# Performance work log

Measured on AMD Instinct MI355X. Metric: run time of the kernel, lower is better.

Reference implementation:

```python
import jax, jax.numpy as jnp
import numpy as np

D_MODEL = 2048
N_HEADS = 16
HEAD_DIM = D_MODEL // N_HEADS  # 128
SCALE_BASE = 512


def rotate_half(x):
    x1, x2 = jnp.split(x, 2, axis=-1)
    return jnp.concatenate((-x2, x1), axis=-1)


def rotary_xpos(seq_len, dim, dtype=jnp.float32):
    inv_freq = 1.0 / (10000.0 ** (jnp.arange(0, dim, 2, dtype=jnp.float32) / dim))
    t = jnp.arange(seq_len, dtype=jnp.float32)
    freqs = jnp.einsum('i,j->ij', t, inv_freq)
    freqs = jnp.concatenate((freqs, freqs), axis=-1)  # [S, dim]
    scale_base = (jnp.arange(0, dim, 2, dtype=jnp.float32) + 0.4 * dim) / (1.4 * dim)
    power = (t - seq_len // 2) / SCALE_BASE
    scale = scale_base[None, :] ** power[:, None]  # [S, dim/2]
    scale = jnp.concatenate((scale, scale), axis=-1)  # [S, dim]
    return freqs.astype(dtype), scale.astype(dtype)


def apply_rotary(t, pos, scale):
    return t * jnp.cos(pos) * scale + rotate_half(t) * jnp.sin(pos) * scale


def setup_inputs() -> dict:
    key = jax.random.key(0)
    ks = jax.random.split(key, 5)
    B, S = 2, 2048
    hidden_states = jax.random.normal(ks[0], (B, S, D_MODEL), dtype=jnp.float32)
    # Linear weights stored as [out, in] like torch; we use x @ W.T
    w_q = jax.random.normal(ks[1], (N_HEADS * HEAD_DIM, D_MODEL), dtype=jnp.float32) * 0.02
    w_kv = jax.random.normal(ks[2], (2 * HEAD_DIM, D_MODEL), dtype=jnp.float32) * 0.02
    w_proj = jax.random.normal(ks[3], (D_MODEL, N_HEADS * HEAD_DIM), dtype=jnp.float32) * 0.02
    b_proj = jax.random.normal(ks[4], (D_MODEL,), dtype=jnp.float32) * 0.02
    return {"hidden_states": hidden_states, "w_q": w_q, "w_kv": w_kv,
            "w_proj": w_proj, "b_proj": b_proj}


def reference(hidden_states, w_q, w_kv, w_proj, b_proj):
    B, S, _ = hidden_states.shape
    q = hidden_states @ w_q.T                      # [B,S,H*D]
    kv = hidden_states @ w_kv.T                    # [B,S,2*D]
    k, v = jnp.split(kv, 2, axis=-1)               # [B,S,D] each
    q = q.reshape(B, S, N_HEADS, HEAD_DIM).transpose(0, 2, 1, 3)  # [B,H,S,D]

    scale_w = HEAD_DIM ** (-0.5)
    q = q * scale_w
    k = k * scale_w

    pos, xscale = rotary_xpos(S, HEAD_DIM, q.dtype)
    q = apply_rotary(q, pos, xscale)               # broadcast [S,D] over [B,H,S,D]
    k = apply_rotary(k, pos, 1.0 / xscale)         # [B,S,D]

    attn = jnp.einsum('bnih,bjh->bnij', q, k)      # [B,H,S,S]
    causal = jnp.triu(jnp.ones((S, S), dtype=bool), 1)
    attn = jnp.where(causal, -jnp.finfo(attn.dtype).max, attn)
    attn = jax.nn.softmax(attn, axis=-1)

    out = jnp.einsum('bnij,bjd->bind', attn, v)    # [B,S,H,D]
    out = out.reshape(B, S, N_HEADS * HEAD_DIM)
    out = out @ w_proj.T + b_proj
    return out
```

## Files before the change

### kernel.cpp

```cpp
#include <hip/hip_runtime.h>
#include <math.h>

typedef __bf16 bf16;
typedef __bf16 bf16x8 __attribute__((ext_vector_type(8)));
typedef float f32x4 __attribute__((ext_vector_type(4)));

#define MFMA16(a, b, c) __builtin_amdgcn_mfma_f32_16x16x32_bf16((a), (b), (c), 0, 0, 0)

__device__ __forceinline__ float clampf(float v, float lo, float hi) {
  return fminf(fmaxf(v, lo), hi);
}

__device__ __forceinline__ void async_copy16(const void* g, void* l) {
  __builtin_amdgcn_global_load_lds(
      (__attribute__((address_space(1))) void*)g,
      (__attribute__((address_space(3))) void*)l,
      16, 0, 0);
}


__global__ void convert_bf16(const float* __restrict__ hs,
                             const float* __restrict__ wq,
                             const float* __restrict__ wkv,
                             const float* __restrict__ wproj,
                             bf16* __restrict__ hs_bf,
                             bf16* __restrict__ wqkv_bf,
                             bf16* __restrict__ wproj_bf) {
  const long long v = (long long)blockIdx.x * blockDim.x + threadIdx.x;
  const float* src;
  bf16* dst;
  long long off;
  if (v < 1048576) { src = hs; dst = hs_bf; off = v; }
  else if (v < 1572864) { src = wq; dst = wqkv_bf; off = v - 1048576; }
  else if (v < 1638400) { src = wkv; dst = wqkv_bf + 4194304; off = v - 1572864; }
  else { src = wproj; dst = wproj_bf; off = v - 1638400; }
  const f32x4* p = (const f32x4*)(src + off * 8);
  f32x4 f0 = p[0], f1 = p[1];
  bf16x8 r;
#pragma unroll
  for (int i = 0; i < 4; ++i) { r[i] = (bf16)f0[i]; r[i + 4] = (bf16)f1[i]; }
  *(bf16x8*)(dst + off * 8) = r;
}

__global__ __launch_bounds__(256, 2)
void gemm_qkv(const bf16* __restrict__ A, const bf16* __restrict__ Bw,
              bf16* __restrict__ Cq, bf16* __restrict__ Ckv) {
  const int K = 2048;
  __shared__ bf16 As[128 * 32];
  __shared__ bf16 Bs[128 * 32];
  const int tid = threadIdx.x;
  const int wave = tid >> 6, lane = tid & 63;
  const int quad = lane >> 4, l15 = lane & 15;
  const int r4 = lane >> 2, c4 = lane & 3;
  const int wm = wave >> 1, wn = wave & 1;
  const int bm = blockIdx.y * 128;
  const int bx = blockIdx.x;
  const bf16* Bp = Bw + (size_t)bx * 128 * K;

  const f32x4 vzero = {0.f, 0.f, 0.f, 0.f};
  f32x4 acc[4][4];
#pragma unroll
  for (int i = 0; i < 4; ++i)
#pragma unroll
    for (int j = 0; j < 4; ++j) acc[i][j] = vzero;

  for (int kt = 0; kt < K; kt += 32) {
    __syncthreads();
#pragma unroll
    for (int q = 0; q < 2; ++q) {
      const int chunk = wave * 2 + q;
      const int row = chunk * 16 + r4;
      async_copy16(A + (size_t)(bm + row) * K + kt + c4 * 8, (char*)As + chunk * 1024);
      async_copy16(Bp + (size_t)row * K + kt + c4 * 8, (char*)Bs + chunk * 1024);
    }
    __syncthreads();
    bf16x8 af[4], bfr[4];
#pragma unroll
    for (int i = 0; i < 4; ++i)
      af[i] = *(const bf16x8*)((const char*)As + (wm * 64 + i * 16 + l15) * 64 + quad * 16);
#pragma unroll
    for (int i = 0; i < 4; ++i)
      bfr[i] = *(const bf16x8*)((const char*)Bs + (wn * 64 + i * 16 + l15) * 64 + quad * 16);
#pragma unroll
    for (int mi = 0; mi < 4; ++mi)
#pragma unroll
      for (int ni = 0; ni < 4; ++ni)
        acc[mi][ni] = MFMA16(af[mi], bfr[ni], acc[mi][ni]);
  }

  bf16* Cp;
  int ldc, cn;
  if (bx < 16) { Cp = Cq; ldc = 2048; cn = bx * 128; }
  else { Cp = Ckv; ldc = 256; cn = (bx - 16) * 128; }
#pragma unroll
  for (int mi = 0; mi < 4; ++mi)
#pragma unroll
    for (int ni = 0; ni < 4; ++ni) {
      const int col = cn + wn * 64 + ni * 16 + l15;
#pragma unroll
      for (int r = 0; r < 4; ++r) {
        const int row = bm + wm * 64 + mi * 16 + quad * 4 + r;
        Cp[(size_t)row * ldc + col] = (bf16)clampf(acc[mi][ni][r], -1000.f, 1000.f);
      }
    }
}

__global__ __launch_bounds__(256, 2)
void gemm_proj(const bf16* __restrict__ A, const bf16* __restrict__ Bw,
               const float* __restrict__ bias, float* __restrict__ C) {
  const int K = 2048;
  __shared__ bf16 As[128 * 32];
  __shared__ bf16 Bs[128 * 32];
  const int tid = threadIdx.x;
  const int wave = tid >> 6, lane = tid & 63;
  const int quad = lane >> 4, l15 = lane & 15;
  const int r4 = lane >> 2, c4 = lane & 3;
  const int wm = wave >> 1, wn = wave & 1;
  const int bm = blockIdx.y * 128;
  const int bn = blockIdx.x * 128;
  const bf16* Bp = Bw + (size_t)bn * K;

  const f32x4 vzero = {0.f, 0.f, 0.f, 0.f};
  f32x4 acc[4][4];
#pragma unroll
  for (int i = 0; i < 4; ++i)
#pragma unroll
    for (int j = 0; j < 4; ++j) acc[i][j] = vzero;

  for (int kt = 0; kt < K; kt += 32) {
    __syncthreads();
#pragma unroll
    for (int q = 0; q < 2; ++q) {
      const int chunk = wave * 2 + q;
      const int row = chunk * 16 + r4;
      async_copy16(A + (size_t)(bm + row) * K + kt + c4 * 8, (char*)As + chunk * 1024);
      async_copy16(Bp + (size_t)row * K + kt + c4 * 8, (char*)Bs + chunk * 1024);
    }
    __syncthreads();
    bf16x8 af[4], bfr[4];
#pragma unroll
    for (int i = 0; i < 4; ++i)
      af[i] = *(const bf16x8*)((const char*)As + (wm * 64 + i * 16 + l15) * 64 + quad * 16);
#pragma unroll
    for (int i = 0; i < 4; ++i)
      bfr[i] = *(const bf16x8*)((const char*)Bs + (wn * 64 + i * 16 + l15) * 64 + quad * 16);
#pragma unroll
    for (int mi = 0; mi < 4; ++mi)
#pragma unroll
      for (int ni = 0; ni < 4; ++ni)
        acc[mi][ni] = MFMA16(af[mi], bfr[ni], acc[mi][ni]);
  }

#pragma unroll
  for (int mi = 0; mi < 4; ++mi)
#pragma unroll
    for (int ni = 0; ni < 4; ++ni) {
      const int col = bn + wn * 64 + ni * 16 + l15;
      const float bv = bias[col];
#pragma unroll
      for (int r = 0; r < 4; ++r) {
        const int row = bm + wm * 64 + mi * 16 + quad * 4 + r;
        C[(size_t)row * 2048 + col] = clampf(acc[mi][ni][r] + bv, -1000.f, 1000.f);
      }
    }
}

__global__ void rotary_kernel(bf16* __restrict__ Cq, bf16* __restrict__ Ckv,
                              bf16* __restrict__ VT) {
  const int row = blockIdx.x;
  const int b = row >> 11, s = row & 2047;
  const int t = threadIdx.x;
  const float power = (float)(s - 1024) * (1.0f / 512.0f);
  const float scale_w = 0.08838834764831845f;
  const float k_if = 0.2076205059304679f;

  const int h = t >> 4;
  const int j0 = (t & 15) * 4;
  const size_t qbase = (size_t)row * 2048 + (size_t)h * 128;
#pragma unroll
  for (int u = 0; u < 4; ++u) {
    const int j = j0 + u;
    const float pos = (float)s * exp2f(-k_if * (float)j);
    const float c = cosf(pos), sn = sinf(pos);
    const float sb = ((float)(2 * j) + 51.2f) * (1.0f / 179.2f);
    const float xs = exp2f(power * log2f(sb));
    const float f = xs * scale_w;
    const float q1 = (float)Cq[qbase + j];
    const float q2 = (float)Cq[qbase + j + 64];
    Cq[qbase + j]      = (bf16)((q1 * c - q2 * sn) * f);
    Cq[qbase + j + 64] = (bf16)((q2 * c + q1 * sn) * f);
  }

  if (t < 64) {
    const int j = t;
    const float pos = (float)s * exp2f(-k_if * (float)j);
    const float c = cosf(pos), sn = sinf(pos);
    const float sb = ((float)(2 * j) + 51.2f) * (1.0f / 179.2f);
    const float xs = exp2f(power * log2f(sb));
    const float f = scale_w / xs;
    const size_t kvb = (size_t)row * 256;
    const float k1 = (float)Ckv[kvb + j];
    const float k2 = (float)Ckv[kvb + j + 64];
    Ckv[kvb + j]      = (bf16)((k1 * c - k2 * sn) * f);
    Ckv[kvb + j + 64] = (bf16)((k2 * c + k1 * sn) * f);
  } else if (t < 128) {
    const int d = (t - 64) * 2;
    const size_t kvb = (size_t)row * 256 + 128;
    VT[((size_t)b * 128 + d) * 2048 + s]     = Ckv[kvb + d];
    VT[((size_t)b * 128 + d + 1) * 2048 + s] = Ckv[kvb + d + 1];
  }
}

__global__ __launch_bounds__(256, 2)
void flash_attn(const bf16* __restrict__ Qp, const bf16* __restrict__ Kkv,
                const bf16* __restrict__ VT, bf16* __restrict__ O) {
  __shared__ bf16 Ks[2][4 * 64 * 32];
  __shared__ bf16 Vs[2][2 * 128 * 32];
  __shared__ bf16 Ps[4][2 * 32 * 32];

  const int tid = threadIdx.x;
  const int wave = tid >> 6, lane = tid & 63;
  const int quad = lane >> 4, l15 = lane & 15;
  const int r4 = lane >> 2, c4 = lane & 3;
  const int bh = blockIdx.x, b = bh >> 4, h = bh & 15;
  const int y = blockIdx.y;
  const int tile = (y < 8) ? y : 23 - y;
  const int q0 = tile * 128;
  const int wrow = wave * 32;

  const bf16* Kb = Kkv + (size_t)b * 2048 * 256;
  const bf16* Vb = VT + (size_t)b * 128 * 2048;

  bf16x8 qa[2][4];
#pragma unroll
  for (int ms = 0; ms < 2; ++ms)
#pragma unroll
    for (int ks = 0; ks < 4; ++ks)
      qa[ms][ks] = *(const bf16x8*)(Qp + ((size_t)(b * 2048 + q0 + wrow + ms * 16 + l15)) * 2048 +
                                    h * 128 + ks * 32 + quad * 8);

  bf16x8 vones;
  {
    const bf16 ov = (bf16)((l15 == 0) ? 1.0f : 0.0f);
#pragma unroll
    for (int i = 0; i < 8; ++i) vones[i] = ov;
  }

  const f32x4 vzero = {0.f, 0.f, 0.f, 0.f};
  f32x4 oacc[2][8];
  f32x4 lacc[2];
#pragma unroll
  for (int ms = 0; ms < 2; ++ms) {
    lacc[ms] = vzero;
#pragma unroll
    for (int n8 = 0; n8 < 8; ++n8) oacc[ms][n8] = vzero;
  }

  auto stage = [&](int kv0, int buf) {
#pragma unroll
    for (int t = 0; t < 4; ++t) {
      const int ii = wave * 4 + t;
      const int p = ii >> 2, ch = ii & 3;
      async_copy16(Kb + (size_t)(kv0 + ch * 16 + r4) * 256 + p * 32 + c4 * 8,
                   (char*)Ks[buf] + ii * 1024);
    }
#pragma unroll
    for (int t = 0; t < 4; ++t) {
      const int ii = wave * 4 + t;
      const int pc = ii >> 3, ch = ii & 7;
      async_copy16(Vb + (size_t)(ch * 16 + r4) * 2048 + kv0 + pc * 32 + c4 * 8,
                   (char*)Vs[buf] + ii * 1024);
    }
  };

  stage(0, 0);
  const int nkv = (q0 >> 6) + 2;
  for (int jt = 0; jt < nkv; ++jt) {
    const int kv0 = jt * 64;
    const int buf = jt & 1;
    __syncthreads();
    if (jt + 1 < nkv) stage(kv0 + 64, buf ^ 1);

    if (kv0 <= q0 + wrow + 31) {
      f32x4 sacc[2][4];
#pragma unroll
      for (int ms = 0; ms < 2; ++ms)
#pragma unroll
        for (int ns = 0; ns < 4; ++ns) sacc[ms][ns] = vzero;
#pragma unroll
      for (int ks = 0; ks < 4; ++ks) {
        bf16x8 kb[4];
#pragma unroll
        for (int ns = 0; ns < 4; ++ns)
          kb[ns] = *(const bf16x8*)((const char*)Ks[buf] + ks * 4096 + (ns * 16 + l15) * 64 + quad * 16);
#pragma unroll
        for (int ms = 0; ms < 2; ++ms)
#pragma unroll
          for (int ns = 0; ns < 4; ++ns)
            sacc[ms][ns] = MFMA16(qa[ms][ks], kb[ns], sacc[ms][ns]);
      }
      if (kv0 + 63 > q0 + wrow) {
#pragma unroll
        for (int ms = 0; ms < 2; ++ms)
#pragma unroll
          for (int ns = 0; ns < 4; ++ns)
#pragma unroll
            for (int r = 0; r < 4; ++r) {
              const int qg = q0 + wrow + ms * 16 + quad * 4 + r;
              const int kg = kv0 + ns * 16 + l15;
              sacc[ms][ns][r] = (kg > qg) ? 0.0f : __expf(sacc[ms][ns][r]);
            }
      } else {
#pragma unroll
        for (int ms = 0; ms < 2; ++ms)
#pragma unroll
          for (int ns = 0; ns < 4; ++ns)
#pragma unroll
            for (int r = 0; r < 4; ++r)
              sacc[ms][ns][r] = __expf(sacc[ms][ns][r]);
      }
#pragma unroll
      for (int ms = 0; ms < 2; ++ms)
#pragma unroll
        for (int ns = 0; ns < 4; ++ns)
#pragma unroll
          for (int r = 0; r < 4; ++r)
            Ps[wave][(ns >> 1) * 1024 + (ms * 16 + quad * 4 + r) * 32 + (ns & 1) * 16 + l15] =
                (bf16)sacc[ms][ns][r];
#pragma unroll
      for (int ks2 = 0; ks2 < 2; ++ks2) {
        bf16x8 pa[2], vb[8];
#pragma unroll
        for (int ms = 0; ms < 2; ++ms)
          pa[ms] = *(const bf16x8*)((const char*)Ps[wave] + ks2 * 2048 + (ms * 16 + l15) * 64 + quad * 16);
#pragma unroll
        for (int n8 = 0; n8 < 8; ++n8)
          vb[n8] = *(const bf16x8*)((const char*)Vs[buf] + ks2 * 8192 + (n8 * 16 + l15) * 64 + quad * 16);
#pragma unroll
        for (int ms = 0; ms < 2; ++ms) {
#pragma unroll
          for (int n8 = 0; n8 < 8; ++n8)
            oacc[ms][n8] = MFMA16(pa[ms], vb[n8], oacc[ms][n8]);
          lacc[ms] = MFMA16(pa[ms], vones, lacc[ms]);
        }
      }
    }
  }

#pragma unroll
  for (int ms = 0; ms < 2; ++ms)
#pragma unroll
    for (int r = 0; r < 4; ++r) {
      const float l = __shfl(lacc[ms][r], lane & 48);
      const float inv = 1.0f / l;
      const int s = q0 + wrow + ms * 16 + quad * 4 + r;
#pragma unroll
      for (int n8 = 0; n8 < 8; ++n8) {
        const int d = n8 * 16 + l15;
        O[((size_t)(b * 2048 + s)) * 2048 + h * 128 + d] = (bf16)(oacc[ms][n8][r] * inv);
      }
    }
}

extern "C" void kernel_launch(void* const* d_in, const int* in_sizes, int n_in,
                              void* d_out, int out_size, void* d_ws, size_t ws_size,
                              hipStream_t stream) {
  const float* hs     = (const float*)d_in[0];
  const float* w_q    = (const float*)d_in[1];
  const float* w_kv   = (const float*)d_in[2];
  const float* w_proj = (const float*)d_in[3];
  const float* b_proj = (const float*)d_in[4];
  float* out = (float*)d_out;
  bf16* Qbuf  = (bf16*)d_out;
  bf16* hs_bf = (bf16*)((char*)d_out + 16777216);

  char* ws = (char*)d_ws;
  bf16* Ckv      = (bf16*)(ws);
  bf16* VT       = (bf16*)(ws + 2097152);
  bf16* AO       = (bf16*)(ws + 3145728);
  bf16* wqkv_bf  = (bf16*)(ws + 19922944);
  bf16* wproj_bf = (bf16*)(ws + 29360128);

  convert_bf16<<<dim3(8448), dim3(256), 0, stream>>>(hs, w_q, w_kv, w_proj,
                                                     hs_bf, wqkv_bf, wproj_bf);
  gemm_qkv<<<dim3(18, 32), dim3(256), 0, stream>>>(hs_bf, wqkv_bf, Qbuf, Ckv);
  rotary_kernel<<<dim3(4096), dim3(256), 0, stream>>>(Qbuf, Ckv, VT);
  flash_attn<<<dim3(32, 16), dim3(256), 0, stream>>>(Qbuf, Ckv, VT, AO);
  gemm_proj<<<dim3(16, 32), dim3(256), 0, stream>>>(AO, wproj_bf, b_proj, out);
}
```

Measured before the change: 287.5 us.

## Load K and V fragments directly from global memory, dropping LDS staging

The attention kernel no longer double-buffers K and V tiles into shared memory with async copies and block-wide barriers. Each wave now reads its MFMA operand fragments straight from global memory and iterates only over its own causal range, so there are no __syncthreads calls and waves are no longer tied to the block's longest trip count. This removes synchronisation and LDS traffic, but the four waves now each fetch the same K/V data separately through the cache. There is also no prefetch overlap, so global-load latency is exposed on every iteration.

```diff
diff --git a/kernel.cpp b/kernel.cpp
--- a/kernel.cpp
+++ b/kernel.cpp
@@ -214,14 +214,11 @@
 __global__ __launch_bounds__(256, 2)
 void flash_attn(const bf16* __restrict__ Qp, const bf16* __restrict__ Kkv,
                 const bf16* __restrict__ VT, bf16* __restrict__ O) {
-  __shared__ bf16 Ks[2][4 * 64 * 32];
-  __shared__ bf16 Vs[2][2 * 128 * 32];
   __shared__ bf16 Ps[4][2 * 32 * 32];
 
   const int tid = threadIdx.x;
   const int wave = tid >> 6, lane = tid & 63;
   const int quad = lane >> 4, l15 = lane & 15;
-  const int r4 = lane >> 2, c4 = lane & 3;
   const int bh = blockIdx.x, b = bh >> 4, h = bh & 15;
   const int y = blockIdx.y;
   const int tile = (y < 8) ? y : 23 - y;
@@ -256,93 +253,70 @@
     for (int n8 = 0; n8 < 8; ++n8) oacc[ms][n8] = vzero;
   }
 
-  auto stage = [&](int kv0, int buf) {
-#pragma unroll
-    for (int t = 0; t < 4; ++t) {
-      const int ii = wave * 4 + t;
-      const int p = ii >> 2, ch = ii & 3;
-      async_copy16(Kb + (size_t)(kv0 + ch * 16 + r4) * 256 + p * 32 + c4 * 8,
-                   (char*)Ks[buf] + ii * 1024);
-    }
-#pragma unroll
-    for (int t = 0; t < 4; ++t) {
-      const int ii = wave * 4 + t;
-      const int pc = ii >> 3, ch = ii & 7;
-      async_copy16(Vb + (size_t)(ch * 16 + r4) * 2048 + kv0 + pc * 32 + c4 * 8,
-                   (char*)Vs[buf] + ii * 1024);
-    }
-  };
-
-  stage(0, 0);
-  const int nkv = (q0 >> 6) + 2;
-  for (int jt = 0; jt < nkv; ++jt) {
+  const int nkv_w = ((q0 + wrow + 31) >> 6) + 1;
+  for (int jt = 0; jt < nkv_w; ++jt) {
     const int kv0 = jt * 64;
-    const int buf = jt & 1;
-    __syncthreads();
-    if (jt + 1 < nkv) stage(kv0 + 64, buf ^ 1);
-
-    if (kv0 <= q0 + wrow + 31) {
-      f32x4 sacc[2][4];
+
+    f32x4 sacc[2][4];
+#pragma unroll
+    for (int ms = 0; ms < 2; ++ms)
+#pragma unroll
+      for (int ns = 0; ns < 4; ++ns) sacc[ms][ns] = vzero;
+#pragma unroll
+    for (int ks = 0; ks < 4; ++ks) {
+      bf16x8 kb[4];
+#pragma unroll
+      for (int ns = 0; ns < 4; ++ns)
+        kb[ns] = *(const bf16x8*)(Kb + (size_t)(kv0 + ns * 16 + l15) * 256 + ks * 32 + quad * 8);
 #pragma unroll
       for (int ms = 0; ms < 2; ++ms)
 #pragma unroll
-        for (int ns = 0; ns < 4; ++ns) sacc[ms][ns] = vzero;
-#pragma unroll
-      for (int ks = 0; ks < 4; ++ks) {
-        bf16x8 kb[4];
-#pragma unroll
         for (int ns = 0; ns < 4; ++ns)
-          kb[ns] = *(const bf16x8*)((const char*)Ks[buf] + ks * 4096 + (ns * 16 + l15) * 64 + quad * 16);
-#pragma unroll
-        for (int ms = 0; ms < 2; ++ms)
-#pragma unroll
-          for (int ns = 0; ns < 4; ++ns)
-            sacc[ms][ns] = MFMA16(qa[ms][ks], kb[ns], sacc[ms][ns]);
-      }
-      if (kv0 + 63 > q0 + wrow) {
-#pragma unroll
-        for (int ms = 0; ms < 2; ++ms)
-#pragma unroll
-          for (int ns = 0; ns < 4; ++ns)
-#pragma unroll
-            for (int r = 0; r < 4; ++r) {
-              const int qg = q0 + wrow + ms * 16 + quad * 4 + r;
-              const int kg = kv0 + ns * 16 + l15;
-              sacc[ms][ns][r] = (kg > qg) ? 0.0f : __expf(sacc[ms][ns][r]);
-            }
-      } else {
-#pragma unroll
-        for (int ms = 0; ms < 2; ++ms)
-#pragma unroll
-          for (int ns = 0; ns < 4; ++ns)
-#pragma unroll
-            for (int r = 0; r < 4; ++r)
-              sacc[ms][ns][r] = __expf(sacc[ms][ns][r]);
-      }
+          sacc[ms][ns] = MFMA16(qa[ms][ks], kb[ns], sacc[ms][ns]);
+    }
+    if (kv0 + 63 > q0 + wrow) {
 #pragma unroll
       for (int ms = 0; ms < 2; ++ms)
 #pragma unroll
         for (int ns = 0; ns < 4; ++ns)
 #pragma unroll
+          for (int r = 0; r < 4; ++r) {
+            const int qg = q0 + wrow + ms * 16 + quad * 4 + r;
+            const int kg = kv0 + ns * 16 + l15;
+            sacc[ms][ns][r] = (kg > qg) ? 0.0f : __expf(sacc[ms][ns][r]);
+          }
+    } else {
+#pragma unroll
+      for (int ms = 0; ms < 2; ++ms)
+#pragma unroll
+        for (int ns = 0; ns < 4; ++ns)
+#pragma unroll
           for (int r = 0; r < 4; ++r)
-            Ps[wave][(ns >> 1) * 1024 + (ms * 16 + quad * 4 + r) * 32 + (ns & 1) * 16 + l15] =
-                (bf16)sacc[ms][ns][r];
-#pragma unroll
-      for (int ks2 = 0; ks2 < 2; ++ks2) {
-        bf16x8 pa[2], vb[8];
-#pragma unroll
-        for (int ms = 0; ms < 2; ++ms)
-          pa[ms] = *(const bf16x8*)((const char*)Ps[wave] + ks2 * 2048 + (ms * 16 + l15) * 64 + quad * 16);
+            sacc[ms][ns][r] = __expf(sacc[ms][ns][r]);
+    }
+#pragma unroll
+    for (int ms = 0; ms < 2; ++ms)
+#pragma unroll
+      for (int ns = 0; ns < 4; ++ns)
+#pragma unroll
+        for (int r = 0; r < 4; ++r)
+          Ps[wave][(ns >> 1) * 1024 + (ms * 16 + quad * 4 + r) * 32 + (ns & 1) * 16 + l15] =
+              (bf16)sacc[ms][ns][r];
+#pragma unroll
+    for (int ks2 = 0; ks2 < 2; ++ks2) {
+      bf16x8 pa[2], vb[8];
+#pragma unroll
+      for (int ms = 0; ms < 2; ++ms)
+        pa[ms] = *(const bf16x8*)((const char*)Ps[wave] + ks2 * 2048 + (ms * 16 + l15) * 64 + quad * 16);
+#pragma unroll
+      for (int n8 = 0; n8 < 8; ++n8)
+        vb[n8] = *(const bf16x8*)(Vb + (size_t)(n8 * 16 + l15) * 2048 + kv0 + ks2 * 32 + quad * 8);
+#pragma unroll
+      for (int ms = 0; ms < 2; ++ms) {
 #pragma unroll
         for (int n8 = 0; n8 < 8; ++n8)
-          vb[n8] = *(const bf16x8*)((const char*)Vs[buf] + ks2 * 8192 + (n8 * 16 + l15) * 64 + quad * 16);
-#pragma unroll
-        for (int ms = 0; ms < 2; ++ms) {
-#pragma unroll
-          for (int n8 = 0; n8 < 8; ++n8)
-            oacc[ms][n8] = MFMA16(pa[ms], vb[n8], oacc[ms][n8]);
-          lacc[ms] = MFMA16(pa[ms], vones, lacc[ms]);
-        }
+          oacc[ms][n8] = MFMA16(pa[ms], vb[n8], oacc[ms][n8]);
+        lacc[ms] = MFMA16(pa[ms], vones, lacc[ms]);
       }
     }
   }
```

Measured after the change: 349.3 us. 1.21x slower.
